# Kernel optimization log

Hardware: AMD Instinct MI355X
Metric: run time of the kernel (lower is better)

## Reference

```python
import jax, jax.numpy as jnp
import numpy as np

B, S, V, D, H, E, A, L = 64, 1024, 32000, 1024, 1024, 1024, 1024, 2


def setup_inputs() -> dict:
    key = jax.random.key(0)
    ks = jax.random.split(key, 24)
    s = 0.02
    d = {}
    d["input_step"] = jax.random.randint(ks[0], (B, 1), 0, V)
    d["h0"] = jax.random.normal(ks[1], (L, B, H), jnp.float32)
    d["c0"] = jax.random.normal(ks[2], (L, B, H), jnp.float32)
    d["encoder_outputs"] = jax.random.normal(ks[3], (B, S, E), jnp.float32)
    # embedding table
    d["emb"] = jax.random.normal(ks[4], (V, D), jnp.float32) * s
    # Bahdanau attention: W1 (decoder hidden -> A), W2 (encoder -> A), v (A -> 1)
    d["Wa_h"] = jax.random.normal(ks[5], (A, H), jnp.float32) * s
    d["ba_h"] = jnp.zeros((A,), jnp.float32)
    d["Wa_e"] = jax.random.normal(ks[6], (A, E), jnp.float32) * s
    d["ba_e"] = jnp.zeros((A,), jnp.float32)
    d["va"] = jax.random.normal(ks[7], (A,), jnp.float32) * s
    d["bva"] = jnp.zeros((), jnp.float32)
    # LSTM layer 0: input dim D+E, gates [i,f,g,o] packed as 4H (PyTorch order)
    d["Wih0"] = jax.random.normal(ks[8], (4 * H, D + E), jnp.float32) * s
    d["Whh0"] = jax.random.normal(ks[9], (4 * H, H), jnp.float32) * s
    d["bih0"] = jnp.zeros((4 * H,), jnp.float32)
    d["bhh0"] = jnp.zeros((4 * H,), jnp.float32)
    # LSTM layer 1: input dim H
    d["Wih1"] = jax.random.normal(ks[10], (4 * H, H), jnp.float32) * s
    d["Whh1"] = jax.random.normal(ks[11], (4 * H, H), jnp.float32) * s
    d["bih1"] = jnp.zeros((4 * H,), jnp.float32)
    d["bhh1"] = jnp.zeros((4 * H,), jnp.float32)
    # output projection
    d["Wout"] = jax.random.normal(ks[12], (V, H), jnp.float32) * s
    d["bout"] = jnp.zeros((V,), jnp.float32)
    return d


def _lstm_cell(x, h, c, Wih, Whh, bih, bhh):
    gates = x @ Wih.T + h @ Whh.T + bih + bhh  # [B, 4H]
    i, f, g, o = jnp.split(gates, 4, axis=-1)  # PyTorch gate order i,f,g,o
    c_new = jax.nn.sigmoid(f) * c + jax.nn.sigmoid(i) * jnp.tanh(g)
    h_new = jax.nn.sigmoid(o) * jnp.tanh(c_new)
    return h_new, c_new


def reference(input_step, h0, c0, encoder_outputs, emb, Wa_h, ba_h, Wa_e, ba_e,
              va, bva, Wih0, Whh0, bih0, bhh0, Wih1, Whh1, bih1, bhh1, Wout, bout):
    # embedding lookup: [B,1] -> [B,D]
    embedded = emb[input_step[:, 0]]
    # Bahdanau attention using top decoder layer hidden state h0[-1]
    q = h0[-1] @ Wa_h.T + ba_h                                   # [B,A]
    k = jnp.einsum('bse,ae->bsa', encoder_outputs, Wa_e) + ba_e  # [B,S,A]
    score = jnp.einsum('bsa,a->bs', jnp.tanh(q[:, None, :] + k), va) + bva
    attn_w = jax.nn.softmax(score, axis=1)                       # [B,S]
    context = jnp.einsum('bs,bse->be', attn_w, encoder_outputs)  # [B,E]
    x = jnp.concatenate([embedded, context], axis=-1)            # [B,D+E]
    # 2-layer LSTM, single time step (inference: no inter-layer dropout)
    h1, c1 = _lstm_cell(x, h0[0], c0[0], Wih0, Whh0, bih0, bhh0)
    h2, c2 = _lstm_cell(h1, h0[1], c0[1], Wih1, Whh1, bih1, bhh1)
    logits = h2 @ Wout.T + bout                                  # [B,V]
    h_new = jnp.stack([h1, h2])
    c_new = jnp.stack([c1, c2])
    return logits, h_new, c_new, attn_w
```

## Files before the change

kernel.cpp:

```cpp
#include <hip/hip_runtime.h>


typedef __attribute__((ext_vector_type(8))) __bf16 bf16x8;
typedef __attribute__((ext_vector_type(4))) __bf16 bf16x4v;
typedef __attribute__((ext_vector_type(4))) float f32x4;

#define GLOADLDS(g, l)                                                         \
  __builtin_amdgcn_global_load_lds(                                            \
      (const __attribute__((address_space(1))) unsigned int*)(g),              \
      (__attribute__((address_space(3))) unsigned int*)(l), 16, 0, 0)

__device__ __forceinline__ ushort4 cvt4(f32x4 v) {
  bf16x4v h = {(__bf16)v.x, (__bf16)v.y, (__bf16)v.z, (__bf16)v.w};
  union { bf16x4v h; ushort4 u; } c; c.h = h; return c.u;
}
__device__ __forceinline__ float bf2f(unsigned short u) {
  return __uint_as_float(((unsigned int)u) << 16);
}
__device__ __forceinline__ float sigm(float x) { return 1.0f / (1.0f + __expf(-x)); }

__global__ __launch_bounds__(256) void cvt_bf_k(const float* __restrict__ in,
                                                unsigned short* __restrict__ out, int n8) {
  int i = blockIdx.x * 256 + threadIdx.x;
  if (i >= n8) return;
  const f32x4* p = (const f32x4*)in + 2 * (size_t)i;
  ushort4* o = (ushort4*)out + 2 * (size_t)i;
  f32x4 a = p[0], b = p[1];
  o[0] = cvt4(a);
  o[1] = cvt4(b);
}

__global__ __launch_bounds__(256) void gather_k(const int* __restrict__ step,
                                                const float* __restrict__ emb,
                                                float* __restrict__ x) {
  int b = blockIdx.x, t = threadIdx.x;
  int row = step[b];
  f32x4 v = *(const f32x4*)(emb + (size_t)row * 1024 + t * 4);
  *(f32x4*)(x + (size_t)b * 2048 + t * 4) = v;
}

__global__ __launch_bounds__(256) void small_gemm(
    const float* __restrict__ A0, int lda0,
    const float* __restrict__ A1, int lda1, int kSplitA,
    const float* __restrict__ B0, int ldb0,
    const float* __restrict__ B1, int ldb1, int kSplitB,
    float* __restrict__ part, int N, int kChunk) {
  __shared__ unsigned short As[64 * 32];
  __shared__ unsigned short Bs[256 * 32];
  int tid = threadIdx.x;
  int n0 = blockIdx.x * 256;
  int k0 = blockIdx.y * kChunk;
  int wave = tid >> 6, lane = tid & 63, quad = lane >> 4, l15 = lane & 15;
  f32x4 acc[4][4] = {};
  for (int kb = k0; kb < k0 + kChunk; kb += 32) {
    const float* Ap; int ldA, kA;
    if (kb < kSplitA) { Ap = A0; ldA = lda0; kA = kb; }
    else              { Ap = A1; ldA = lda1; kA = kb - kSplitA; }
    const float* Bp; int ldB, kB;
    if (kb < kSplitB) { Bp = B0; ldB = ldb0; kB = kb; }
    else              { Bp = B1; ldB = ldb1; kB = kb - kSplitB; }
#pragma unroll
    for (int c = 0; c < 2; c++) {
      int f = c * 256 + tid;
      int row = f >> 3, colf = f & 7;
      f32x4 v = *(const f32x4*)(Ap + (size_t)row * ldA + kA + colf * 4);
      *(ushort4*)&As[row * 32 + colf * 4] = cvt4(v);
    }
#pragma unroll
    for (int c = 0; c < 8; c++) {
      int f = c * 256 + tid;
      int row = f >> 3, colf = f & 7;
      f32x4 v = *(const f32x4*)(Bp + (size_t)(n0 + row) * ldB + kB + colf * 4);
      *(ushort4*)&Bs[row * 32 + colf * 4] = cvt4(v);
    }
    __syncthreads();
    bf16x8 af[4], bfv[4];
#pragma unroll
    for (int rt = 0; rt < 4; rt++)
      af[rt] = *(const bf16x8*)&As[(16 * rt + l15) * 32 + quad * 8];
#pragma unroll
    for (int ct = 0; ct < 4; ct++)
      bfv[ct] = *(const bf16x8*)&Bs[(64 * wave + 16 * ct + l15) * 32 + quad * 8];
#pragma unroll
    for (int rt = 0; rt < 4; rt++)
#pragma unroll
      for (int ct = 0; ct < 4; ct++)
        acc[rt][ct] = __builtin_amdgcn_mfma_f32_16x16x32_bf16(af[rt], bfv[ct], acc[rt][ct], 0, 0, 0);
    __syncthreads();
  }
  size_t base = (size_t)blockIdx.y * 64 * (size_t)N;
#pragma unroll
  for (int rt = 0; rt < 4; rt++)
#pragma unroll
    for (int ct = 0; ct < 4; ct++)
#pragma unroll
      for (int r = 0; r < 4; r++) {
        int m = 16 * rt + 4 * quad + r;
        int n = n0 + 64 * wave + 16 * ct + l15;
        part[base + (size_t)m * N + n] = acc[rt][ct][r];
      }
}

__global__ __launch_bounds__(256) void q_reduce(const float* __restrict__ qpart,
                                                const float* __restrict__ ba_h,
                                                float* __restrict__ q) {
  int idx = blockIdx.x * 256 + threadIdx.x;
  int a = idx & 1023;
  float s = ba_h[a];
#pragma unroll
  for (int sp = 0; sp < 8; sp++) s += qpart[sp * 65536 + idx];
  q[idx] = s;
}

__global__ __launch_bounds__(512) void attn_gemm_bf(
    const unsigned short* __restrict__ encb, const unsigned short* __restrict__ Waeb,
    const float* __restrict__ q, const float* __restrict__ ba_e,
    const float* __restrict__ va, float* __restrict__ score) {
  __shared__ unsigned short As[128 * 32];
  __shared__ unsigned short Bs[256 * 32];
  __shared__ float red[128];
  int tid = threadIdx.x;
  int n0 = blockIdx.x * 256, m0 = blockIdx.y * 128;
  int wave = tid >> 6, lane = tid & 63, quad = lane >> 4, l15 = lane & 15;
  int wr = wave >> 2, wc = wave & 3;
  int lr = lane >> 2, lc = lane & 3;
  const unsigned short* ga = encb + (size_t)(m0 + 16 * wave + lr) * 1024 + lc * 8;
  const unsigned short* gb = Waeb + (size_t)(n0 + 32 * wave + lr) * 1024 + lc * 8;
  unsigned short* lA  = &As[wave * 512];
  unsigned short* lB0 = &Bs[wave * 1024];
  unsigned short* lB1 = &Bs[wave * 1024 + 512];
  f32x4 acc[4][4] = {};
  for (int kb = 0; kb < 1024; kb += 32) {
    GLOADLDS(ga + kb, lA);
    GLOADLDS(gb + kb, lB0);
    GLOADLDS(gb + kb + 16 * 1024, lB1);
    __syncthreads();
    bf16x8 af[4], bfv[4];
#pragma unroll
    for (int rt = 0; rt < 4; rt++)
      af[rt] = *(const bf16x8*)&As[(64 * wr + 16 * rt + l15) * 32 + quad * 8];
#pragma unroll
    for (int ct = 0; ct < 4; ct++)
      bfv[ct] = *(const bf16x8*)&Bs[(64 * wc + 16 * ct + l15) * 32 + quad * 8];
#pragma unroll
    for (int rt = 0; rt < 4; rt++)
#pragma unroll
      for (int ct = 0; ct < 4; ct++)
        acc[rt][ct] = __builtin_amdgcn_mfma_f32_16x16x32_bf16(af[rt], bfv[ct], acc[rt][ct], 0, 0, 0);
    __syncthreads();
  }
  int b = m0 >> 10;
  if (tid < 128) red[tid] = 0.0f;
  __syncthreads();
  float qe[4], vv[4];
#pragma unroll
  for (int ct = 0; ct < 4; ct++) {
    int n = n0 + 64 * wc + 16 * ct + l15;
    qe[ct] = q[b * 1024 + n] + ba_e[n];
    vv[ct] = va[n];
  }
#pragma unroll
  for (int rt = 0; rt < 4; rt++)
#pragma unroll
    for (int r = 0; r < 4; r++) {
      float p = 0.0f;
#pragma unroll
      for (int ct = 0; ct < 4; ct++)
        p += vv[ct] * tanhf(qe[ct] + acc[rt][ct][r]);
      p += __shfl_xor(p, 1); p += __shfl_xor(p, 2);
      p += __shfl_xor(p, 4); p += __shfl_xor(p, 8);
      if (l15 == 0) atomicAdd(&red[64 * wr + 16 * rt + 4 * quad + r], p);
    }
  __syncthreads();
  if (tid < 128) atomicAdd(&score[m0 + tid], red[tid]);
}

__global__ __launch_bounds__(512) void attn_gemm_f32(
    const float* __restrict__ enc, const float* __restrict__ Wae,
    const float* __restrict__ q, const float* __restrict__ ba_e,
    const float* __restrict__ va, float* __restrict__ score) {
  __shared__ unsigned short As[128 * 32];
  __shared__ unsigned short Bs[256 * 32];
  __shared__ float red[128];
  int tid = threadIdx.x;
  int n0 = blockIdx.x * 256, m0 = blockIdx.y * 128;
  int wave = tid >> 6, lane = tid & 63, quad = lane >> 4, l15 = lane & 15;
  int wr = wave >> 2, wc = wave & 3;
  f32x4 acc[4][4] = {};
  for (int kb = 0; kb < 1024; kb += 32) {
#pragma unroll
    for (int c = 0; c < 2; c++) {
      int f = c * 512 + tid;
      int row = f >> 3, colf = f & 7;
      f32x4 v = *(const f32x4*)(enc + (size_t)(m0 + row) * 1024 + kb + colf * 4);
      *(ushort4*)&As[row * 32 + colf * 4] = cvt4(v);
    }
#pragma unroll
    for (int c = 0; c < 4; c++) {
      int f = c * 512 + tid;
      int row = f >> 3, colf = f & 7;
      f32x4 v = *(const f32x4*)(Wae + (size_t)(n0 + row) * 1024 + kb + colf * 4);
      *(ushort4*)&Bs[row * 32 + colf * 4] = cvt4(v);
    }
    __syncthreads();
    bf16x8 af[4], bfv[4];
#pragma unroll
    for (int rt = 0; rt < 4; rt++)
      af[rt] = *(const bf16x8*)&As[(64 * wr + 16 * rt + l15) * 32 + quad * 8];
#pragma unroll
    for (int ct = 0; ct < 4; ct++)
      bfv[ct] = *(const bf16x8*)&Bs[(64 * wc + 16 * ct + l15) * 32 + quad * 8];
#pragma unroll
    for (int rt = 0; rt < 4; rt++)
#pragma unroll
      for (int ct = 0; ct < 4; ct++)
        acc[rt][ct] = __builtin_amdgcn_mfma_f32_16x16x32_bf16(af[rt], bfv[ct], acc[rt][ct], 0, 0, 0);
    __syncthreads();
  }
  int b = m0 >> 10;
  if (tid < 128) red[tid] = 0.0f;
  __syncthreads();
  float qe[4], vv[4];
#pragma unroll
  for (int ct = 0; ct < 4; ct++) {
    int n = n0 + 64 * wc + 16 * ct + l15;
    qe[ct] = q[b * 1024 + n] + ba_e[n];
    vv[ct] = va[n];
  }
#pragma unroll
  for (int rt = 0; rt < 4; rt++)
#pragma unroll
    for (int r = 0; r < 4; r++) {
      float p = 0.0f;
#pragma unroll
      for (int ct = 0; ct < 4; ct++)
        p += vv[ct] * tanhf(qe[ct] + acc[rt][ct][r]);
      p += __shfl_xor(p, 1); p += __shfl_xor(p, 2);
      p += __shfl_xor(p, 4); p += __shfl_xor(p, 8);
      if (l15 == 0) atomicAdd(&red[64 * wr + 16 * rt + 4 * quad + r], p);
    }
  __syncthreads();
  if (tid < 128) atomicAdd(&score[m0 + tid], red[tid]);
}

__global__ __launch_bounds__(256) void softmax_k(const float* __restrict__ score,
                                                 float* __restrict__ attnw) {
  int b = blockIdx.x, tid = threadIdx.x;
  __shared__ float wred[4];
  float v[4];
  float mx = -1e30f;
#pragma unroll
  for (int i = 0; i < 4; i++) {
    v[i] = score[b * 1024 + tid + 256 * i];
    mx = fmaxf(mx, v[i]);
  }
  for (int off = 1; off < 64; off <<= 1) mx = fmaxf(mx, __shfl_xor(mx, off));
  int w = tid >> 6;
  if ((tid & 63) == 0) wred[w] = mx;
  __syncthreads();
  mx = fmaxf(fmaxf(wred[0], wred[1]), fmaxf(wred[2], wred[3]));
  float s = 0.0f;
#pragma unroll
  for (int i = 0; i < 4; i++) { v[i] = __expf(v[i] - mx); s += v[i]; }
  for (int off = 1; off < 64; off <<= 1) s += __shfl_xor(s, off);
  __syncthreads();
  if ((tid & 63) == 0) wred[w] = s;
  __syncthreads();
  s = wred[0] + wred[1] + wred[2] + wred[3];
  float inv = 1.0f / s;
#pragma unroll
  for (int i = 0; i < 4; i++) attnw[b * 1024 + tid + 256 * i] = v[i] * inv;
}

__global__ __launch_bounds__(256) void context_bf(const unsigned short* __restrict__ encb,
                                                  const float* __restrict__ attnw,
                                                  float* __restrict__ ctxpart) {
  int b = blockIdx.x, sc = blockIdx.y, tid = threadIdx.x;
  __shared__ float w[128];
  if (tid < 128) w[tid] = attnw[b * 1024 + sc * 128 + tid];
  __syncthreads();
  const unsigned short* ep = encb + (size_t)b * 1048576 + (size_t)sc * 128 * 1024 + tid * 4;
  f32x4 a0 = {}, a1 = {};
  for (int s = 0; s < 128; s += 2) {
    ushort4 u0 = *(const ushort4*)(ep + (size_t)s * 1024);
    ushort4 u1 = *(const ushort4*)(ep + (size_t)(s + 1) * 1024);
    float w0 = w[s], w1 = w[s + 1];
    a0.x += w0 * bf2f(u0.x); a0.y += w0 * bf2f(u0.y);
    a0.z += w0 * bf2f(u0.z); a0.w += w0 * bf2f(u0.w);
    a1.x += w1 * bf2f(u1.x); a1.y += w1 * bf2f(u1.y);
    a1.z += w1 * bf2f(u1.z); a1.w += w1 * bf2f(u1.w);
  }
  f32x4 r = a0 + a1;
  *(f32x4*)(ctxpart + ((size_t)sc * 64 + b) * 1024 + tid * 4) = r;
}

__global__ __launch_bounds__(256) void ctx_reduce(const float* __restrict__ ctxpart,
                                                  float* __restrict__ x) {
  int idx = blockIdx.x * 256 + threadIdx.x;
  int b = idx >> 10, e = idx & 1023;
  float s = 0.0f;
#pragma unroll
  for (int sc = 0; sc < 8; sc++) s += ctxpart[((size_t)sc * 64 + b) * 1024 + e];
  x[(size_t)b * 2048 + 1024 + e] = s;
}

__global__ __launch_bounds__(256) void context_k(const float* __restrict__ enc,
                                                 const float* __restrict__ attnw,
                                                 float* __restrict__ x) {
  __shared__ float w[1024];
  int b = blockIdx.y, e0 = blockIdx.x * 256, tid = threadIdx.x;
#pragma unroll
  for (int i = 0; i < 4; i++) w[tid + 256 * i] = attnw[b * 1024 + tid + 256 * i];
  __syncthreads();
  const float* ep = enc + (size_t)b * 1024 * 1024 + e0 + tid;
  float acc = 0.0f;
#pragma unroll 4
  for (int s = 0; s < 1024; s++) acc += w[s] * ep[(size_t)s * 1024];
  x[(size_t)b * 2048 + 1024 + e0 + tid] = acc;
}

__global__ __launch_bounds__(256) void cell_k(const float* __restrict__ part, int nsplit,
                                              const float* __restrict__ bih,
                                              const float* __restrict__ bhh,
                                              const float* __restrict__ cin,
                                              float* __restrict__ hout,
                                              float* __restrict__ cout) {
  int idx = blockIdx.x * 256 + threadIdx.x;
  int b = idx >> 10, h = idx & 1023;
  float gi = bih[h] + bhh[h];
  float gf = bih[1024 + h] + bhh[1024 + h];
  float gg = bih[2048 + h] + bhh[2048 + h];
  float go = bih[3072 + h] + bhh[3072 + h];
  const float* p = part + (size_t)b * 4096 + h;
  for (int sp = 0; sp < nsplit; sp++, p += 262144) {
    gi += p[0]; gf += p[1024]; gg += p[2048]; go += p[3072];
  }
  float c = sigm(gf) * cin[idx] + sigm(gi) * tanhf(gg);
  float hh = sigm(go) * tanhf(c);
  cout[idx] = c;
  hout[idx] = hh;
}

__global__ __launch_bounds__(256) void logits_reduce(const float* __restrict__ part,
                                                     const float* __restrict__ bout,
                                                     float* __restrict__ out) {
  int v = blockIdx.x * 256 + threadIdx.x;
  int b = blockIdx.y;
  size_t i = (size_t)b * 32000 + v;
  out[i] = bout[v] + part[i] + part[2048000 + i];
}

extern "C" void kernel_launch(void* const* d_in, const int* in_sizes, int n_in,
                              void* d_out, int out_size, void* d_ws, size_t ws_size,
                              hipStream_t stream) {
  const int*   input_step = (const int*)d_in[0];
  const float* h0   = (const float*)d_in[1];
  const float* c0   = (const float*)d_in[2];
  const float* enc  = (const float*)d_in[3];
  const float* emb  = (const float*)d_in[4];
  const float* Wa_h = (const float*)d_in[5];
  const float* ba_h = (const float*)d_in[6];
  const float* Wa_e = (const float*)d_in[7];
  const float* ba_e = (const float*)d_in[8];
  const float* va   = (const float*)d_in[9];
  const float* Wih0 = (const float*)d_in[11];
  const float* Whh0 = (const float*)d_in[12];
  const float* bih0 = (const float*)d_in[13];
  const float* bhh0 = (const float*)d_in[14];
  const float* Wih1 = (const float*)d_in[15];
  const float* Whh1 = (const float*)d_in[16];
  const float* bih1 = (const float*)d_in[17];
  const float* bhh1 = (const float*)d_in[18];
  const float* Wout = (const float*)d_in[19];
  const float* bout = (const float*)d_in[20];

  float* out    = (float*)d_out;
  float* logits = out;
  float* h1o    = out + 2048000;
  float* h2o    = out + 2113536;
  float* c1o    = out + 2179072;
  float* c2o    = out + 2244608;
  float* attnw  = out + 2310144;

  float* ws      = (float*)d_ws;
  float* x       = ws;
  float* q       = ws + 131072;
  float* score   = ws + 196608;
  float* part    = ws + 262144;
  float* ctxpart = ws + 4358144;
  unsigned short* Waeb = (unsigned short*)(ws + 4882432);
  unsigned short* encb = (unsigned short*)(ws + 6979584);
  const bool big = ws_size >= 162136064ull;

  gather_k<<<64, 256, 0, stream>>>(input_step, emb, x);

  small_gemm<<<dim3(4, 8), 256, 0, stream>>>(
      h0 + 65536, 1024, h0 + 65536, 1024, 1024,
      Wa_h, 1024, Wa_h, 1024, 1024,
      part, 1024, 128);
  q_reduce<<<256, 256, 0, stream>>>(part, ba_h, q);

  hipMemsetAsync(score, 0, 65536 * sizeof(float), stream);

  if (big) {
    cvt_bf_k<<<512, 256, 0, stream>>>(Wa_e, Waeb, 131072);
    cvt_bf_k<<<32768, 256, 0, stream>>>(enc, encb, 8388608);
    attn_gemm_bf<<<dim3(4, 512), 512, 0, stream>>>(encb, Waeb, q, ba_e, va, score);
    softmax_k<<<64, 256, 0, stream>>>(score, attnw);
    context_bf<<<dim3(64, 8), 256, 0, stream>>>(encb, attnw, ctxpart);
    ctx_reduce<<<256, 256, 0, stream>>>(ctxpart, x);
  } else {
    attn_gemm_f32<<<dim3(4, 512), 512, 0, stream>>>(enc, Wa_e, q, ba_e, va, score);
    softmax_k<<<64, 256, 0, stream>>>(score, attnw);
    context_k<<<dim3(4, 64), 256, 0, stream>>>(enc, attnw, x);
  }

  small_gemm<<<dim3(16, 12), 256, 0, stream>>>(
      x, 2048, h0, 1024, 2048,
      Wih0, 2048, Whh0, 1024, 2048,
      part, 4096, 256);
  cell_k<<<256, 256, 0, stream>>>(part, 12, bih0, bhh0, c0, h1o, c1o);

  small_gemm<<<dim3(16, 8), 256, 0, stream>>>(
      h1o, 1024, h0 + 65536, 1024, 1024,
      Wih1, 1024, Whh1, 1024, 1024,
      part, 4096, 256);
  cell_k<<<256, 256, 0, stream>>>(part, 8, bih1, bhh1, c0 + 65536, h2o, c2o);

  small_gemm<<<dim3(125, 2), 256, 0, stream>>>(
      h2o, 1024, h2o, 1024, 1024,
      Wout, 1024, Wout, 1024, 1024,
      part, 32000, 512);
  logits_reduce<<<dim3(125, 64), 256, 0, stream>>>(part, bout, logits);
}
```

Before: 853.0 us.

## Rewrite attention score GEMM as double-buffered 256x256 pipelined MFMA kernel

Replaces the 128x256-tile attention GEMM with a 256x256-tile kernel using K=64 stages, double-buffered LDS staging via global_load_lds, XOR-swizzled LDS layout, explicit barrier/waitcnt phases with setprio around MFMA groups, and a grouped block-to-tile mapping for L2 reuse. It also swaps tanhf for an exp-based fast tanh in the epilogue. The aim is to hide global load latency behind MFMA work and raise arithmetic intensity. In exchange it uses 128KB of LDS and hand-tuned scheduling that depends on exact vmcnt counts, and the fast tanh loses some precision.

```diff
diff --git a/kernel.cpp b/kernel.cpp
--- a/kernel.cpp
+++ b/kernel.cpp
@@ -18,6 +18,9 @@
   return __uint_as_float(((unsigned int)u) << 16);
 }
 __device__ __forceinline__ float sigm(float x) { return 1.0f / (1.0f + __expf(-x)); }
+__device__ __forceinline__ float fast_tanh(float x) {
+  return 1.0f - 2.0f / (__expf(2.0f * x) + 1.0f);
+}
 
 __global__ __launch_bounds__(256) void cvt_bf_k(const float* __restrict__ in,
                                                 unsigned short* __restrict__ out, int n8) {
@@ -112,68 +115,165 @@
   q[idx] = s;
 }
 
-__global__ __launch_bounds__(512) void attn_gemm_bf(
+
+#define SCHED0() __builtin_amdgcn_sched_barrier(0)
+
+#define STAGE_TILE(t)                                                        \
+  {                                                                          \
+    int _buf = (t) & 1;                                                      \
+    const unsigned short* _as = encb + aSrc + (size_t)(t) * 64;              \
+    const unsigned short* _bs = Waeb + bSrc + (size_t)(t) * 64;              \
+    unsigned short* _la = &sh[_buf * 32768 + wave * 512];                    \
+    unsigned short* _lb = &sh[_buf * 32768 + 16384 + wave * 512];            \
+    GLOADLDS(_as,          _la);                                             \
+    GLOADLDS(_as + 65536,  _la + 4096);                                      \
+    GLOADLDS(_as + 131072, _la + 8192);                                      \
+    GLOADLDS(_as + 196608, _la + 12288);                                     \
+    GLOADLDS(_bs,          _lb);                                             \
+    GLOADLDS(_bs + 65536,  _lb + 4096);                                      \
+    GLOADLDS(_bs + 131072, _lb + 8192);                                      \
+    GLOADLDS(_bs + 196608, _lb + 12288);                                     \
+  }
+
+#define LOAD_A(buf, mh)                                                      \
+  {                                                                          \
+    const unsigned short* _p = &sh[(buf) * 32768 + aRow + (mh) * 4096];      \
+    _Pragma("unroll") for (int mr = 0; mr < 4; mr++) {                       \
+      a[mr][0] = *(const bf16x8*)&_p[mr * 1024 + cs0];                       \
+      a[mr][1] = *(const bf16x8*)&_p[mr * 1024 + cs1];                       \
+    }                                                                        \
+  }
+
+#define LOAD_B(buf, nh, Bd)                                                  \
+  {                                                                          \
+    const unsigned short* _p = &sh[(buf) * 32768 + 16384 + bRow + (nh) * 2048]; \
+    _Pragma("unroll") for (int nc = 0; nc < 2; nc++) {                       \
+      Bd[nc][0] = *(const bf16x8*)&_p[nc * 1024 + cs0];                      \
+      Bd[nc][1] = *(const bf16x8*)&_p[nc * 1024 + cs1];                      \
+    }                                                                        \
+  }
+
+#define MMQ(mh, nh, Bd)                                                      \
+  _Pragma("unroll") for (int mr = 0; mr < 4; mr++)                           \
+  _Pragma("unroll") for (int nc = 0; nc < 2; nc++)                           \
+  _Pragma("unroll") for (int ks = 0; ks < 2; ks++)                           \
+    acc[(mh) * 4 + mr][(nh) * 2 + nc] = __builtin_amdgcn_mfma_f32_16x16x32_bf16( \
+        a[mr][ks], Bd[nc][ks], acc[(mh) * 4 + mr][(nh) * 2 + nc], 0, 0, 0);
+
+#define PH_WAIT_LGKM()                                                       \
+  SCHED0();                                                                  \
+  __builtin_amdgcn_s_barrier();                                              \
+  asm volatile("s_waitcnt lgkmcnt(0)" ::: "memory");                         \
+  SCHED0();
+
+#define PH_END()                                                             \
+  SCHED0();                                                                  \
+  __builtin_amdgcn_s_barrier();                                              \
+  SCHED0();
+
+#define GROUP(c, MODE)                                                       \
+  {                                                                          \
+    int buf = (c) & 1;                                                       \
+                    \
+    LOAD_A(buf, 0);                                                          \
+    LOAD_B(buf, 0, b0);                                                      \
+    PH_WAIT_LGKM();                                                          \
+    __builtin_amdgcn_s_setprio(1); MMQ(0, 0, b0); __builtin_amdgcn_s_setprio(0); \
+    PH_END();                                                                \
+                                      \
+    LOAD_B(buf, 1, b1);                                                      \
+    PH_WAIT_LGKM();                                                          \
+    __builtin_amdgcn_s_setprio(1); MMQ(0, 1, b1); __builtin_amdgcn_s_setprio(0); \
+    PH_END();                                                                \
+                                      \
+    LOAD_A(buf, 1);                                                          \
+    PH_WAIT_LGKM();                                                          \
+    __builtin_amdgcn_s_setprio(1); MMQ(1, 0, b0); __builtin_amdgcn_s_setprio(0); \
+    PH_END();                                                                \
+     \
+    if ((MODE) == 0) { STAGE_TILE((c) + 2); }                                \
+    if ((MODE) == 0) asm volatile("s_waitcnt vmcnt(8)" ::: "memory");        \
+    if ((MODE) == 1) asm volatile("s_waitcnt vmcnt(0)" ::: "memory");        \
+    SCHED0();                                                                \
+    __builtin_amdgcn_s_barrier();                                            \
+    SCHED0();                                                                \
+    __builtin_amdgcn_s_setprio(1); MMQ(1, 1, b1); __builtin_amdgcn_s_setprio(0); \
+    PH_END();                                                                \
+  }
+
+__global__ __launch_bounds__(512, 2) void attn_gemm_8p(
     const unsigned short* __restrict__ encb, const unsigned short* __restrict__ Waeb,
     const float* __restrict__ q, const float* __restrict__ ba_e,
     const float* __restrict__ va, float* __restrict__ score) {
-  __shared__ unsigned short As[128 * 32];
-  __shared__ unsigned short Bs[256 * 32];
-  __shared__ float red[128];
+  __shared__ unsigned short sh[65536];
+  __shared__ float red[256];
   int tid = threadIdx.x;
-  int n0 = blockIdx.x * 256, m0 = blockIdx.y * 128;
   int wave = tid >> 6, lane = tid & 63, quad = lane >> 4, l15 = lane & 15;
   int wr = wave >> 2, wc = wave & 3;
-  int lr = lane >> 2, lc = lane & 3;
-  const unsigned short* ga = encb + (size_t)(m0 + 16 * wave + lr) * 1024 + lc * 8;
-  const unsigned short* gb = Waeb + (size_t)(n0 + 32 * wave + lr) * 1024 + lc * 8;
-  unsigned short* lA  = &As[wave * 512];
-  unsigned short* lB0 = &Bs[wave * 1024];
-  unsigned short* lB1 = &Bs[wave * 1024 + 512];
-  f32x4 acc[4][4] = {};
-  for (int kb = 0; kb < 1024; kb += 32) {
-    GLOADLDS(ga + kb, lA);
-    GLOADLDS(gb + kb, lB0);
-    GLOADLDS(gb + kb + 16 * 1024, lB1);
-    __syncthreads();
-    bf16x8 af[4], bfv[4];
-#pragma unroll
-    for (int rt = 0; rt < 4; rt++)
-      af[rt] = *(const bf16x8*)&As[(64 * wr + 16 * rt + l15) * 32 + quad * 8];
-#pragma unroll
-    for (int ct = 0; ct < 4; ct++)
-      bfv[ct] = *(const bf16x8*)&Bs[(64 * wc + 16 * ct + l15) * 32 + quad * 8];
-#pragma unroll
-    for (int rt = 0; rt < 4; rt++)
-#pragma unroll
-      for (int ct = 0; ct < 4; ct++)
-        acc[rt][ct] = __builtin_amdgcn_mfma_f32_16x16x32_bf16(af[rt], bfv[ct], acc[rt][ct], 0, 0, 0);
-    __syncthreads();
-  }
+
+  int h = blockIdx.y * 4 + blockIdx.x;
+  int lgc = (h & 7) * 128 + (h >> 3);
+  int m0 = (lgc >> 2) * 256, n0 = (lgc & 3) * 256;
+
+  int srow = wave * 8 + (lane >> 3);
+  int sslot = ((lane & 7) ^ (lane >> 3)) * 8;
+  size_t aSrc = (size_t)(m0 + srow) * 1024 + sslot;
+  size_t bSrc = (size_t)(n0 + srow) * 1024 + sslot;
+
+  int aRow = (wr * 128 + l15) * 64;
+  int bRow = (wc * 64 + l15) * 64;
+  int cs0 = (quad ^ (l15 & 7)) * 8;
+  int cs1 = ((4 + quad) ^ (l15 & 7)) * 8;
+
+  bf16x8 a[4][2], b0[2][2], b1[2][2];
+  f32x4 acc[8][4] = {};
+
+  STAGE_TILE(0);
+  STAGE_TILE(1);
+  asm volatile("s_waitcnt vmcnt(8)" ::: "memory");
+  SCHED0();
+  __builtin_amdgcn_s_barrier();
+  SCHED0();
+
+  for (int c = 0; c < 14; ++c) GROUP(c, 0);
+  GROUP(14, 1);
+  GROUP(15, 2);
+
+  __syncthreads();
+  if (tid < 256) red[tid] = 0.0f;
+  __syncthreads();
   int b = m0 >> 10;
-  if (tid < 128) red[tid] = 0.0f;
-  __syncthreads();
   float qe[4], vv[4];
 #pragma unroll
-  for (int ct = 0; ct < 4; ct++) {
-    int n = n0 + 64 * wc + 16 * ct + l15;
-    qe[ct] = q[b * 1024 + n] + ba_e[n];
-    vv[ct] = va[n];
-  }
-#pragma unroll
-  for (int rt = 0; rt < 4; rt++)
+  for (int j = 0; j < 4; j++) {
+    int n = n0 + wc * 64 + j * 16 + l15;
+    qe[j] = q[b * 1024 + n] + ba_e[n];
+    vv[j] = va[n];
+  }
+#pragma unroll
+  for (int i = 0; i < 8; i++)
 #pragma unroll
     for (int r = 0; r < 4; r++) {
       float p = 0.0f;
 #pragma unroll
-      for (int ct = 0; ct < 4; ct++)
-        p += vv[ct] * tanhf(qe[ct] + acc[rt][ct][r]);
+      for (int j = 0; j < 4; j++)
+        p += vv[j] * fast_tanh(qe[j] + acc[i][j][r]);
       p += __shfl_xor(p, 1); p += __shfl_xor(p, 2);
       p += __shfl_xor(p, 4); p += __shfl_xor(p, 8);
-      if (l15 == 0) atomicAdd(&red[64 * wr + 16 * rt + 4 * quad + r], p);
+      if (l15 == 0) atomicAdd(&red[wr * 128 + i * 16 + quad * 4 + r], p);
     }
   __syncthreads();
-  if (tid < 128) atomicAdd(&score[m0 + tid], red[tid]);
-}
+  if (tid < 256) atomicAdd(&score[m0 + tid], red[tid]);
+}
+
+#undef GROUP
+#undef PH_END
+#undef PH_WAIT_LGKM
+#undef MMQ
+#undef LOAD_B
+#undef LOAD_A
+#undef STAGE_TILE
+#undef SCHED0
 
 __global__ __launch_bounds__(512) void attn_gemm_f32(
     const float* __restrict__ enc, const float* __restrict__ Wae,
@@ -405,7 +505,7 @@
   if (big) {
     cvt_bf_k<<<512, 256, 0, stream>>>(Wa_e, Waeb, 131072);
     cvt_bf_k<<<32768, 256, 0, stream>>>(enc, encb, 8388608);
-    attn_gemm_bf<<<dim3(4, 512), 512, 0, stream>>>(encb, Waeb, q, ba_e, va, score);
+    attn_gemm_8p<<<dim3(4, 256), 512, 0, stream>>>(encb, Waeb, q, ba_e, va, score);
     softmax_k<<<64, 256, 0, stream>>>(score, attnw);
     context_bf<<<dim3(64, 8), 256, 0, stream>>>(encb, attnw, ctxpart);
     ctx_reduce<<<256, 256, 0, stream>>>(ctxpart, x);
```

Result: no change. 867.3 us (+1.7%).
